# Performance work log

Measured on AMD Instinct MI355X. Metric: run time of the kernel, lower is better.

Reference implementation:

```python
import jax, jax.numpy as jnp
import numpy as np

N = 50000      # num nodes
E = 400000     # num edges (before self loops)
IN = 128       # in_channels
H = 4          # num_heads
C = 64         # hidden_channels (per head)
NEG_SLOPE = 0.2
BN_EPS = 1e-5


def gatv2_layer(x, Wl, Wr, att, bias, src, dst, n, concat):
    # GATv2Conv (PyG, share_weights=False): xl for source/messages, xr for dest
    h, c = att.shape
    xl = (x @ Wl).reshape(n, h, c)
    xr = (x @ Wr).reshape(n, h, c)
    # per-edge attention logits: [E, H]
    e = jnp.sum(jax.nn.leaky_relu(xl[src] + xr[dst], NEG_SLOPE) * att[None], axis=-1)
    # edge softmax grouped by destination node
    m = jax.ops.segment_max(e, dst, num_segments=n)          # [N, H]
    ex = jnp.exp(e - m[dst])
    den = jax.ops.segment_sum(ex, dst, num_segments=n)       # [N, H]
    alpha = ex / (den[dst] + 1e-16)                          # [E, H]
    # weighted scatter-sum aggregation: [N, H, C]
    out = jax.ops.segment_sum(alpha[..., None] * xl[src], dst, num_segments=n)
    out = out.reshape(n, h * c) if concat else out.mean(axis=1)
    return out + bias


def bn_eval(x, gamma, beta):
    # eval-mode BatchNorm1d with init running stats (mean=0, var=1)
    return x / jnp.sqrt(jnp.asarray(1.0 + BN_EPS, x.dtype)) * gamma + beta


def setup_inputs() -> dict:
    key = jax.random.key(0)
    ks = jax.random.split(key, 20)
    s = 0.05
    return {
        "x": jax.random.normal(ks[0], (N, IN), jnp.float32),
        "edge_index": jax.random.randint(ks[1], (2, E), 0, N, jnp.int32),
        # layer 1: in=128 -> heads=4, out=64, concat -> 256
        "W1l": jax.random.normal(ks[2], (IN, H * C), jnp.float32) * s,
        "W1r": jax.random.normal(ks[3], (IN, H * C), jnp.float32) * s,
        "att1": jax.random.normal(ks[4], (H, C), jnp.float32) * s,
        "b1": jnp.zeros((H * C,), jnp.float32),
        "g1": jnp.ones((H * C,), jnp.float32),
        "be1": jnp.zeros((H * C,), jnp.float32),
        # layer 2: in=256 -> heads=4, out=64, mean -> 64
        "W2l": jax.random.normal(ks[5], (H * C, H * C), jnp.float32) * s,
        "W2r": jax.random.normal(ks[6], (H * C, H * C), jnp.float32) * s,
        "att2": jax.random.normal(ks[7], (H, C), jnp.float32) * s,
        "b2": jnp.zeros((C,), jnp.float32),
        "g2": jnp.ones((C,), jnp.float32),
        "be2": jnp.zeros((C,), jnp.float32),
        # final linear 64 -> 1
        "fcW": jax.random.normal(ks[8], (C, 1), jnp.float32) * s,
        "fcb": jnp.zeros((1,), jnp.float32),
    }


def reference(x, edge_index, W1l, W1r, att1, b1, g1, be1,
              W2l, W2r, att2, b2, g2, be2, fcW, fcb):
    # PyG GATv2Conv adds self loops by default
    loops = jnp.arange(N, dtype=edge_index.dtype)
    src = jnp.concatenate([edge_index[0], loops])
    dst = jnp.concatenate([edge_index[1], loops])

    h = gatv2_layer(x, W1l, W1r, att1, b1, src, dst, N, concat=True)   # [N, 256]
    h = jax.nn.elu(bn_eval(h, g1, be1))                                 # dropout = id (eval)
    h = gatv2_layer(h, W2l, W2r, att2, b2, src, dst, N, concat=False)  # [N, 64]
    h = jax.nn.elu(bn_eval(h, g2, be2))
    out = jax.nn.sigmoid(h @ fcW + fcb)                                 # [N, 1]
    return out
```

## Files before the change

### kernel.cpp

```cpp
#include <hip/hip_runtime.h>
#include <math.h>

#define NNODES 50000
#define NEDGES 400000
#define E2 (NEDGES + NNODES)
#define HC 256
#define NOUT 512
#define NF (NOUT / 16)
#define BN_SCALE 0.9999950000374997f
#define SCAN_B ((NNODES + 255) / 256)

typedef unsigned short ushortx8 __attribute__((ext_vector_type(8)));
typedef __bf16 bf16x8 __attribute__((ext_vector_type(8)));
typedef float f32x4 __attribute__((ext_vector_type(4)));
typedef float f32x2 __attribute__((ext_vector_type(2)));

__device__ inline unsigned short f2bf(float f) {
    unsigned u = __float_as_uint(f);
    u += 0x7fff + ((u >> 16) & 1);
    return (unsigned short)(u >> 16);
}
__device__ inline float bf2f(unsigned short u) {
    return __uint_as_float(((unsigned)u) << 16);
}

__global__ void hist_dst(const int* __restrict__ ei, int* __restrict__ deg) {
    int i = blockIdx.x * blockDim.x + threadIdx.x;
    if (i >= E2) return;
    int d = (i < NEDGES) ? ei[NEDGES + i] : i - NEDGES;
    atomicAdd(&deg[d], 1);
}

__global__ __launch_bounds__(256) void scan1(const int* __restrict__ deg,
                                             int* __restrict__ rowptr,
                                             int* __restrict__ bsum) {
    int t = threadIdx.x;
    int i = blockIdx.x * 256 + t;
    int v = (i < NNODES) ? deg[i] : 0;
    __shared__ int buf[256];
    buf[t] = v;
    __syncthreads();
    for (int off = 1; off < 256; off <<= 1) {
        int u = (t >= off) ? buf[t - off] : 0;
        __syncthreads();
        buf[t] += u;
        __syncthreads();
    }
    if (i < NNODES) rowptr[i] = buf[t] - v;
    if (t == 255) bsum[blockIdx.x] = buf[255];
}

__global__ __launch_bounds__(256) void scan2(int* __restrict__ bsum,
                                             int* __restrict__ rowptr) {
    int t = threadIdx.x;
    int v = (t < SCAN_B) ? bsum[t] : 0;
    __shared__ int buf[256];
    buf[t] = v;
    __syncthreads();
    for (int off = 1; off < 256; off <<= 1) {
        int u = (t >= off) ? buf[t - off] : 0;
        __syncthreads();
        buf[t] += u;
        __syncthreads();
    }
    if (t < SCAN_B) bsum[t] = buf[t] - v;
    if (t == 0) rowptr[NNODES] = E2;
}

__global__ void scan3(int* __restrict__ rowptr, const int* __restrict__ bsum,
                      int* __restrict__ cursor) {
    int i = blockIdx.x * 256 + threadIdx.x;
    if (i >= NNODES) return;
    int r = rowptr[i] + bsum[blockIdx.x];
    rowptr[i] = r;
    cursor[i] = r;
}

__global__ void scatter_csr(const int* __restrict__ ei, int* __restrict__ cursor,
                            int* __restrict__ csr_src) {
    int i = blockIdx.x * blockDim.x + threadIdx.x;
    if (i >= E2) return;
    int s, d;
    if (i < NEDGES) { s = ei[i]; d = ei[NEDGES + i]; }
    else            { s = i - NEDGES; d = s; }
    int slot = atomicAdd(&cursor[d], 1);
    csr_src[slot] = s;
}

__device__ inline void prep_one(const float* __restrict__ Wl, const float* __restrict__ Wr,
                                unsigned short* __restrict__ Bf, int id) {
    int j    = id & 7;
    int lane = (id >> 3) & 63;
    int nf   = (id >> 9) & (NF - 1);
    int kb   = id >> 14;
    int k = kb * 32 + (lane >> 4) * 8 + j;
    int c = nf * 16 + (lane & 15);
    float v = (c < 256) ? Wl[k * 256 + c] : Wr[k * 256 + (c - 256)];
    Bf[id] = f2bf(v);
}

#define XCVT_N (NNODES * 128 / 4)
#define B1_N (128 * NOUT)
#define B2_N (256 * NOUT)

__global__ void pack_all(const float* __restrict__ x,
                         const float* __restrict__ W1l, const float* __restrict__ W1r,
                         const float* __restrict__ W2l, const float* __restrict__ W2r,
                         unsigned short* __restrict__ x_bf,
                         unsigned short* __restrict__ Bf1,
                         unsigned short* __restrict__ Bf2) {
    int id = blockIdx.x * blockDim.x + threadIdx.x;
    if (id < XCVT_N) {
        float4 v = reinterpret_cast<const float4*>(x)[id];
        ushort4 o = { f2bf(v.x), f2bf(v.y), f2bf(v.z), f2bf(v.w) };
        reinterpret_cast<ushort4*>(x_bf)[id] = o;
    } else if (id < XCVT_N + B1_N) {
        prep_one(W1l, W1r, Bf1, id - XCVT_N);
    } else if (id < XCVT_N + B1_N + B2_N) {
        prep_one(W2l, W2r, Bf2, id - XCVT_N - B1_N);
    }
}

__global__ __launch_bounds__(256) void gemm_mfma(
        const unsigned short* __restrict__ A,
        const unsigned short* __restrict__ Bf,
        unsigned short* __restrict__ C,
        int M, int K) {
    const int tid  = threadIdx.x;
    const int lane = tid & 63;
    const int w    = tid >> 6;
    const int row0 = blockIdx.x * 64;
    const int col0 = w * 128;
    const int lr = lane & 15, lg = lane >> 4;

    f32x4 acc[4][8] = {};
    const int nkb = K >> 5;
    for (int kb = 0; kb < nkb; ++kb) {
        bf16x8 af[4], bfr[8];
        const int kcol = kb * 32 + lg * 8;
#pragma unroll
        for (int i = 0; i < 4; ++i) {
            int r = row0 + i * 16 + lr;
            ushortx8 av = {};
            if (r < M)
                av = *reinterpret_cast<const ushortx8*>(A + (size_t)r * K + kcol);
            af[i] = __builtin_bit_cast(bf16x8, av);
        }
#pragma unroll
        for (int j = 0; j < 8; ++j) {
            int nf = (col0 >> 4) + j;
            ushortx8 bv = *reinterpret_cast<const ushortx8*>(
                Bf + (((size_t)(kb * NF + nf) * 64 + lane) << 3));
            bfr[j] = __builtin_bit_cast(bf16x8, bv);
        }
#pragma unroll
        for (int i = 0; i < 4; ++i)
#pragma unroll
            for (int j = 0; j < 8; ++j)
                acc[i][j] = __builtin_amdgcn_mfma_f32_16x16x32_bf16(
                    af[i], bfr[j], acc[i][j], 0, 0, 0);
    }
#pragma unroll
    for (int i = 0; i < 4; ++i) {
#pragma unroll
        for (int r = 0; r < 4; ++r) {
            int row = row0 + i * 16 + lg * 4 + r;
            if (row < M) {
#pragma unroll
                for (int j = 0; j < 8; ++j)
                    C[(size_t)row * NOUT + col0 + j * 16 + lr] = f2bf(acc[i][j][r]);
            }
        }
    }
}

template <int LAYER>
__global__ __launch_bounds__(256) void gat_node(
        const unsigned short* __restrict__ xlr,
        const float* __restrict__ att, const int* __restrict__ rowptr,
        const int* __restrict__ csr_src,
        const float* __restrict__ bias, const float* __restrict__ g,
        const float* __restrict__ be,
        const float* __restrict__ fcW, const float* __restrict__ fcb,
        void* __restrict__ outv) {
    int wid  = (blockIdx.x * blockDim.x + threadIdx.x) >> 6;
    int lane = threadIdx.x & 63;
    if (wid >= NNODES) return;

    f32x2 xb01, xb23, at01, at23;
    {
        uint2 wv = *reinterpret_cast<const uint2*>(xlr + (size_t)wid * NOUT + 256 + lane * 4);
        xb01.x = __uint_as_float(wv.x << 16);
        xb01.y = __uint_as_float(wv.x & 0xffff0000u);
        xb23.x = __uint_as_float(wv.y << 16);
        xb23.y = __uint_as_float(wv.y & 0xffff0000u);
        float4 a = *reinterpret_cast<const float4*>(att + lane * 4);
        at01.x = a.x; at01.y = a.y;
        at23.x = a.z; at23.y = a.w;
    }
    const int beg = rowptr[wid];
    const int end = rowptr[wid + 1];
    const unsigned short* __restrict__ xbase = xlr + lane * 4;

    float den = 0.f;
    f32x2 ac01 = {0.f, 0.f}, ac23 = {0.f, 0.f};

    auto edge = [&](uint2 wv) {
        f32x2 xv01, xv23;
        xv01.x = __uint_as_float(wv.x << 16);
        xv01.y = __uint_as_float(wv.x & 0xffff0000u);
        xv23.x = __uint_as_float(wv.y << 16);
        xv23.y = __uint_as_float(wv.y & 0xffff0000u);
        f32x2 v01 = xv01 + xb01;
        f32x2 v23 = xv23 + xb23;
        v01 = __builtin_elementwise_max(v01, v01 * 0.2f);
        v23 = __builtin_elementwise_max(v23, v23 * 0.2f);
        f32x2 d2 = v01 * at01 + v23 * at23;
        float part = d2.x + d2.y;
        part += __shfl_xor(part, 1);
        part += __shfl_xor(part, 2);
        part += __shfl_xor(part, 4);
        part += __shfl_xor(part, 8);
        float p = __expf(part);
        den += p;
        ac01 += p * xv01;
        ac23 += p * xv23;
    };

    int j = beg;
    for (; j + 2 <= end; j += 2) {
        int s0 = csr_src[j];
        int s1 = csr_src[j + 1];
        uint2 w0 = *reinterpret_cast<const uint2*>(xbase + (size_t)s0 * NOUT);
        uint2 w1 = *reinterpret_cast<const uint2*>(xbase + (size_t)s1 * NOUT);
        edge(w0);
        edge(w1);
    }
    if (j < end) {
        int s0 = csr_src[j];
        uint2 w0 = *reinterpret_cast<const uint2*>(xbase + (size_t)s0 * NOUT);
        edge(w0);
    }

    float inv = 1.f / (den + 1e-16f);
    float ax = ac01.x * inv, ay = ac01.y * inv, az = ac23.x * inv, aw = ac23.y * inv;

    if (LAYER == 1) {
        int c0 = lane * 4;
        float o0 = (ax + bias[c0 + 0]) * BN_SCALE * g[c0 + 0] + be[c0 + 0];
        float o1 = (ay + bias[c0 + 1]) * BN_SCALE * g[c0 + 1] + be[c0 + 1];
        float o2 = (az + bias[c0 + 2]) * BN_SCALE * g[c0 + 2] + be[c0 + 2];
        float o3 = (aw + bias[c0 + 3]) * BN_SCALE * g[c0 + 3] + be[c0 + 3];
        o0 = o0 > 0.f ? o0 : expm1f(o0);
        o1 = o1 > 0.f ? o1 : expm1f(o1);
        o2 = o2 > 0.f ? o2 : expm1f(o2);
        o3 = o3 > 0.f ? o3 : expm1f(o3);
        ushort4 o = { f2bf(o0), f2bf(o1), f2bf(o2), f2bf(o3) };
        *reinterpret_cast<ushort4*>((unsigned short*)outv + (size_t)wid * HC + lane * 4) = o;
    } else {
#pragma unroll
        for (int off = 16; off < 64; off <<= 1) {
            ax += __shfl_xor(ax, off);
            ay += __shfl_xor(ay, off);
            az += __shfl_xor(az, off);
            aw += __shfl_xor(aw, off);
        }
        int c0 = (lane & 15) * 4;
        float v0 = (ax * 0.25f + bias[c0 + 0]) * BN_SCALE * g[c0 + 0] + be[c0 + 0];
        float v1 = (ay * 0.25f + bias[c0 + 1]) * BN_SCALE * g[c0 + 1] + be[c0 + 1];
        float v2 = (az * 0.25f + bias[c0 + 2]) * BN_SCALE * g[c0 + 2] + be[c0 + 2];
        float v3 = (aw * 0.25f + bias[c0 + 3]) * BN_SCALE * g[c0 + 3] + be[c0 + 3];
        v0 = v0 > 0.f ? v0 : expm1f(v0);
        v1 = v1 > 0.f ? v1 : expm1f(v1);
        v2 = v2 > 0.f ? v2 : expm1f(v2);
        v3 = v3 > 0.f ? v3 : expm1f(v3);
        float dot = v0 * fcW[c0] + v1 * fcW[c0 + 1] + v2 * fcW[c0 + 2] + v3 * fcW[c0 + 3];
#pragma unroll
        for (int off = 8; off; off >>= 1) dot += __shfl_xor(dot, off);
        if (lane == 0) ((float*)outv)[wid] = 1.f / (1.f + __expf(-(dot + fcb[0])));
    }
}

extern "C" void kernel_launch(void* const* d_in, const int* in_sizes, int n_in,
                              void* d_out, int out_size, void* d_ws, size_t ws_size,
                              hipStream_t stream) {
    const float* x    = (const float*)d_in[0];
    const int*   ei   = (const int*)d_in[1];
    const float* W1l  = (const float*)d_in[2];
    const float* W1r  = (const float*)d_in[3];
    const float* att1 = (const float*)d_in[4];
    const float* b1   = (const float*)d_in[5];
    const float* g1   = (const float*)d_in[6];
    const float* be1  = (const float*)d_in[7];
    const float* W2l  = (const float*)d_in[8];
    const float* W2r  = (const float*)d_in[9];
    const float* att2 = (const float*)d_in[10];
    const float* b2   = (const float*)d_in[11];
    const float* g2   = (const float*)d_in[12];
    const float* be2  = (const float*)d_in[13];
    const float* fcW  = (const float*)d_in[14];
    const float* fcb  = (const float*)d_in[15];
    float* out = (float*)d_out;

    unsigned short* xlr   = (unsigned short*)d_ws;
    unsigned short* x_bf  = xlr + (size_t)NNODES * NOUT;
    unsigned short* h1_bf = x_bf + (size_t)NNODES * 128;
    unsigned short* Bf1   = h1_bf + (size_t)NNODES * 256;
    unsigned short* Bf2   = Bf1 + 128 * NOUT;
    int* csr_src = (int*)(Bf2 + 256 * NOUT);
    int* deg     = csr_src + E2;
    int* rowptr  = deg + NNODES;
    int* cursor  = rowptr + NNODES + 1;
    int* bsum    = cursor + NNODES;

    const int edgeBlocks = (E2 + 255) / 256;
    const int nodeBlocks = (NNODES * 64 + 255) / 256;
    const int gemmGrid   = (NNODES + 63) / 64;
    const int packBlocks = (XCVT_N + B1_N + B2_N + 255) / 256;

    hipMemsetAsync(deg, 0, NNODES * sizeof(int), stream);
    hist_dst<<<edgeBlocks, 256, 0, stream>>>(ei, deg);
    scan1<<<SCAN_B, 256, 0, stream>>>(deg, rowptr, bsum);
    scan2<<<1, 256, 0, stream>>>(bsum, rowptr);
    scan3<<<SCAN_B, 256, 0, stream>>>(rowptr, bsum, cursor);
    scatter_csr<<<edgeBlocks, 256, 0, stream>>>(ei, cursor, csr_src);

    pack_all<<<packBlocks, 256, 0, stream>>>(x, W1l, W1r, W2l, W2r, x_bf, Bf1, Bf2);

    gemm_mfma<<<gemmGrid, 256, 0, stream>>>(x_bf, Bf1, xlr, NNODES, 128);
    gat_node<1><<<nodeBlocks, 256, 0, stream>>>(xlr, att1, rowptr, csr_src,
                                                b1, g1, be1, nullptr, nullptr, h1_bf);

    gemm_mfma<<<gemmGrid, 256, 0, stream>>>(h1_bf, Bf2, xlr, NNODES, 256);
    gat_node<2><<<nodeBlocks, 256, 0, stream>>>(xlr, att2, rowptr, csr_src,
                                                b2, g2, be2, fcW, fcb, out);
}
```

Measured before the change: 232.9 us.

## Fuse CSR build into pack/GEMM launches, use DPP reductions, unroll edge loop by 4

Merges the histogram into the pack kernel and the first scan pass into the first GEMM launch using block-index dispatch. It also replaces the separate scan2/scan3 kernels with a single kernel in which each block reduces its preceding block sums. This cuts the number of launches and serial gaps in the setup phase. Separately, it replaces the shuffle-based 16-lane reductions in the GAT node kernels with DPP row operations and unrolls the edge gather loop to four edges for more memory-level parallelism. The costs are higher register pressure and some redundant per-block summation in the scan.

Measured after the change: 208.9 us. 1.11x faster.

```diff
diff --git a/kernel.cpp b/kernel.cpp
--- a/kernel.cpp
+++ b/kernel.cpp
@@ -9,6 +9,8 @@
 #define NF (NOUT / 16)
 #define BN_SCALE 0.9999950000374997f
 #define SCAN_B ((NNODES + 255) / 256)
+#define GEMM_B ((NNODES + 63) / 64)
+#define HIST_B ((E2 + 255) / 256)
 
 typedef unsigned short ushortx8 __attribute__((ext_vector_type(8)));
 typedef __bf16 bf16x8 __attribute__((ext_vector_type(8)));
@@ -20,75 +22,28 @@
     u += 0x7fff + ((u >> 16) & 1);
     return (unsigned short)(u >> 16);
 }
-__device__ inline float bf2f(unsigned short u) {
-    return __uint_as_float(((unsigned)u) << 16);
-}
-
-__global__ void hist_dst(const int* __restrict__ ei, int* __restrict__ deg) {
-    int i = blockIdx.x * blockDim.x + threadIdx.x;
-    if (i >= E2) return;
-    int d = (i < NEDGES) ? ei[NEDGES + i] : i - NEDGES;
-    atomicAdd(&deg[d], 1);
-}
-
-__global__ __launch_bounds__(256) void scan1(const int* __restrict__ deg,
-                                             int* __restrict__ rowptr,
-                                             int* __restrict__ bsum) {
-    int t = threadIdx.x;
-    int i = blockIdx.x * 256 + t;
-    int v = (i < NNODES) ? deg[i] : 0;
-    __shared__ int buf[256];
-    buf[t] = v;
-    __syncthreads();
-    for (int off = 1; off < 256; off <<= 1) {
-        int u = (t >= off) ? buf[t - off] : 0;
-        __syncthreads();
-        buf[t] += u;
-        __syncthreads();
-    }
-    if (i < NNODES) rowptr[i] = buf[t] - v;
-    if (t == 255) bsum[blockIdx.x] = buf[255];
-}
-
-__global__ __launch_bounds__(256) void scan2(int* __restrict__ bsum,
-                                             int* __restrict__ rowptr) {
-    int t = threadIdx.x;
-    int v = (t < SCAN_B) ? bsum[t] : 0;
-    __shared__ int buf[256];
-    buf[t] = v;
-    __syncthreads();
-    for (int off = 1; off < 256; off <<= 1) {
-        int u = (t >= off) ? buf[t - off] : 0;
-        __syncthreads();
-        buf[t] += u;
-        __syncthreads();
-    }
-    if (t < SCAN_B) bsum[t] = buf[t] - v;
-    if (t == 0) rowptr[NNODES] = E2;
-}
-
-__global__ void scan3(int* __restrict__ rowptr, const int* __restrict__ bsum,
-                      int* __restrict__ cursor) {
-    int i = blockIdx.x * 256 + threadIdx.x;
-    if (i >= NNODES) return;
-    int r = rowptr[i] + bsum[blockIdx.x];
-    rowptr[i] = r;
-    cursor[i] = r;
-}
-
-__global__ void scatter_csr(const int* __restrict__ ei, int* __restrict__ cursor,
-                            int* __restrict__ csr_src) {
-    int i = blockIdx.x * blockDim.x + threadIdx.x;
-    if (i >= E2) return;
-    int s, d;
-    if (i < NEDGES) { s = ei[i]; d = ei[NEDGES + i]; }
-    else            { s = i - NEDGES; d = s; }
-    int slot = atomicAdd(&cursor[d], 1);
-    csr_src[slot] = s;
-}
-
-__device__ inline void prep_one(const float* __restrict__ Wl, const float* __restrict__ Wr,
-                                unsigned short* __restrict__ Bf, int id) {
+
+template <int CTRL>
+__device__ __forceinline__ float dpp_add(float x) {
+    int y = __builtin_amdgcn_update_dpp(0, __float_as_int(x), CTRL, 0xF, 0xF, true);
+    return x + __int_as_float(y);
+}
+__device__ __forceinline__ float row16_sum(float x) {
+    x = dpp_add<0xB1>(x);
+    x = dpp_add<0x4E>(x);
+    x = dpp_add<0x141>(x);
+    x = dpp_add<0x140>(x);
+    return x;
+}
+
+#define XCVT_N (NNODES * 128 / 4)
+#define B1_N (128 * NOUT)
+#define B2_N (256 * NOUT)
+#define PACK_B ((XCVT_N + B1_N + B2_N + 255) / 256)
+
+__device__ __forceinline__ void prep_one(const float* __restrict__ Wl,
+                                         const float* __restrict__ Wr,
+                                         unsigned short* __restrict__ Bf, int id) {
     int j    = id & 7;
     int lane = (id >> 3) & 63;
     int nf   = (id >> 9) & (NF - 1);
@@ -99,37 +54,40 @@
     Bf[id] = f2bf(v);
 }
 
-#define XCVT_N (NNODES * 128 / 4)
-#define B1_N (128 * NOUT)
-#define B2_N (256 * NOUT)
-
-__global__ void pack_all(const float* __restrict__ x,
-                         const float* __restrict__ W1l, const float* __restrict__ W1r,
-                         const float* __restrict__ W2l, const float* __restrict__ W2r,
-                         unsigned short* __restrict__ x_bf,
-                         unsigned short* __restrict__ Bf1,
-                         unsigned short* __restrict__ Bf2) {
-    int id = blockIdx.x * blockDim.x + threadIdx.x;
-    if (id < XCVT_N) {
-        float4 v = reinterpret_cast<const float4*>(x)[id];
-        ushort4 o = { f2bf(v.x), f2bf(v.y), f2bf(v.z), f2bf(v.w) };
-        reinterpret_cast<ushort4*>(x_bf)[id] = o;
-    } else if (id < XCVT_N + B1_N) {
-        prep_one(W1l, W1r, Bf1, id - XCVT_N);
-    } else if (id < XCVT_N + B1_N + B2_N) {
-        prep_one(W2l, W2r, Bf2, id - XCVT_N - B1_N);
-    }
-}
-
-__global__ __launch_bounds__(256) void gemm_mfma(
-        const unsigned short* __restrict__ A,
-        const unsigned short* __restrict__ Bf,
-        unsigned short* __restrict__ C,
-        int M, int K) {
-    const int tid  = threadIdx.x;
+__global__ __launch_bounds__(256) void k1_pack_hist(
+        const float* __restrict__ x,
+        const float* __restrict__ W1l, const float* __restrict__ W1r,
+        const float* __restrict__ W2l, const float* __restrict__ W2r,
+        unsigned short* __restrict__ x_bf,
+        unsigned short* __restrict__ Bf1, unsigned short* __restrict__ Bf2,
+        const int* __restrict__ ei, int* __restrict__ deg) {
+    int bid = blockIdx.x;
+    if (bid < PACK_B) {
+        int id = bid * 256 + threadIdx.x;
+        if (id < XCVT_N) {
+            float4 v = reinterpret_cast<const float4*>(x)[id];
+            ushort4 o = { f2bf(v.x), f2bf(v.y), f2bf(v.z), f2bf(v.w) };
+            reinterpret_cast<ushort4*>(x_bf)[id] = o;
+        } else if (id < XCVT_N + B1_N) {
+            prep_one(W1l, W1r, Bf1, id - XCVT_N);
+        } else if (id < XCVT_N + B1_N + B2_N) {
+            prep_one(W2l, W2r, Bf2, id - XCVT_N - B1_N);
+        }
+    } else {
+        int i = (bid - PACK_B) * 256 + threadIdx.x;
+        if (i < E2) {
+            int d = (i < NEDGES) ? ei[NEDGES + i] : i - NEDGES;
+            atomicAdd(&deg[d], 1);
+        }
+    }
+}
+
+__device__ __forceinline__ void gemm_body(int bx, int tid,
+        const unsigned short* __restrict__ A, const unsigned short* __restrict__ Bf,
+        unsigned short* __restrict__ C, int M, int K) {
     const int lane = tid & 63;
     const int w    = tid >> 6;
-    const int row0 = blockIdx.x * 64;
+    const int row0 = bx * 64;
     const int col0 = w * 128;
     const int lr = lane & 15, lg = lane >> 4;
 
@@ -172,6 +130,69 @@
             }
         }
     }
+}
+
+__global__ __launch_bounds__(256) void k2_gemm1_scan1(
+        const unsigned short* __restrict__ A, const unsigned short* __restrict__ Bf,
+        unsigned short* __restrict__ C, int M, int K,
+        const int* __restrict__ deg, int* __restrict__ rowptr, int* __restrict__ bsum) {
+    __shared__ int buf[256];
+    if (blockIdx.x < GEMM_B) {
+        gemm_body(blockIdx.x, threadIdx.x, A, Bf, C, M, K);
+    } else {
+        int bx = blockIdx.x - GEMM_B;
+        int t = threadIdx.x;
+        int i = bx * 256 + t;
+        int v = (i < NNODES) ? deg[i] : 0;
+        buf[t] = v;
+        __syncthreads();
+        for (int off = 1; off < 256; off <<= 1) {
+            int u = (t >= off) ? buf[t - off] : 0;
+            __syncthreads();
+            buf[t] += u;
+            __syncthreads();
+        }
+        if (i < NNODES) rowptr[i] = buf[t] - v;
+        if (t == 255) bsum[bx] = buf[255];
+    }
+}
+
+__global__ __launch_bounds__(256) void k3_scan23(
+        const int* __restrict__ bsum, int* __restrict__ rowptr, int* __restrict__ cursor) {
+    __shared__ int sbuf[256];
+    int t = threadIdx.x;
+    int v = (t < (int)blockIdx.x && t < SCAN_B) ? bsum[t] : 0;
+    sbuf[t] = v;
+    __syncthreads();
+    for (int off = 128; off; off >>= 1) {
+        if (t < off) sbuf[t] += sbuf[t + off];
+        __syncthreads();
+    }
+    int base = sbuf[0];
+    int i = blockIdx.x * 256 + t;
+    if (i < NNODES) {
+        int r = rowptr[i] + base;
+        rowptr[i] = r;
+        cursor[i] = r;
+    }
+    if (blockIdx.x == 0 && t == 0) rowptr[NNODES] = E2;
+}
+
+__global__ __launch_bounds__(256) void k4_scatter(
+        const int* __restrict__ ei, int* __restrict__ cursor, int* __restrict__ csr_src) {
+    int i = blockIdx.x * blockDim.x + threadIdx.x;
+    if (i >= E2) return;
+    int s, d;
+    if (i < NEDGES) { s = ei[i]; d = ei[NEDGES + i]; }
+    else            { s = i - NEDGES; d = s; }
+    int slot = atomicAdd(&cursor[d], 1);
+    csr_src[slot] = s;
+}
+
+__global__ __launch_bounds__(256) void gemm_mfma(
+        const unsigned short* __restrict__ A, const unsigned short* __restrict__ Bf,
+        unsigned short* __restrict__ C, int M, int K) {
+    gemm_body(blockIdx.x, threadIdx.x, A, Bf, C, M, K);
 }
 
 template <int LAYER>
@@ -216,11 +237,7 @@
         v01 = __builtin_elementwise_max(v01, v01 * 0.2f);
         v23 = __builtin_elementwise_max(v23, v23 * 0.2f);
         f32x2 d2 = v01 * at01 + v23 * at23;
-        float part = d2.x + d2.y;
-        part += __shfl_xor(part, 1);
-        part += __shfl_xor(part, 2);
-        part += __shfl_xor(part, 4);
-        part += __shfl_xor(part, 8);
+        float part = row16_sum(d2.x + d2.y);
         float p = __expf(part);
         den += p;
         ac01 += p * xv01;
@@ -228,15 +245,15 @@
     };
 
     int j = beg;
-    for (; j + 2 <= end; j += 2) {
-        int s0 = csr_src[j];
-        int s1 = csr_src[j + 1];
+    for (; j + 4 <= end; j += 4) {
+        int s0 = csr_src[j], s1 = csr_src[j + 1], s2 = csr_src[j + 2], s3 = csr_src[j + 3];
         uint2 w0 = *reinterpret_cast<const uint2*>(xbase + (size_t)s0 * NOUT);
         uint2 w1 = *reinterpret_cast<const uint2*>(xbase + (size_t)s1 * NOUT);
-        edge(w0);
-        edge(w1);
-    }
-    if (j < end) {
+        uint2 w2 = *reinterpret_cast<const uint2*>(xbase + (size_t)s2 * NOUT);
+        uint2 w3 = *reinterpret_cast<const uint2*>(xbase + (size_t)s3 * NOUT);
+        edge(w0); edge(w1); edge(w2); edge(w3);
+    }
+    for (; j < end; ++j) {
         int s0 = csr_src[j];
         uint2 w0 = *reinterpret_cast<const uint2*>(xbase + (size_t)s0 * NOUT);
         edge(w0);
@@ -275,8 +292,7 @@
         v2 = v2 > 0.f ? v2 : expm1f(v2);
         v3 = v3 > 0.f ? v3 : expm1f(v3);
         float dot = v0 * fcW[c0] + v1 * fcW[c0 + 1] + v2 * fcW[c0 + 2] + v3 * fcW[c0 + 3];
-#pragma unroll
-        for (int off = 8; off; off >>= 1) dot += __shfl_xor(dot, off);
+        dot = row16_sum(dot);
         if (lane == 0) ((float*)outv)[wid] = 1.f / (1.f + __expf(-(dot + fcb[0])));
     }
 }
@@ -313,25 +329,24 @@
     int* cursor  = rowptr + NNODES + 1;
     int* bsum    = cursor + NNODES;
 
-    const int edgeBlocks = (E2 + 255) / 256;
     const int nodeBlocks = (NNODES * 64 + 255) / 256;
-    const int gemmGrid   = (NNODES + 63) / 64;
-    const int packBlocks = (XCVT_N + B1_N + B2_N + 255) / 256;
 
     hipMemsetAsync(deg, 0, NNODES * sizeof(int), stream);
-    hist_dst<<<edgeBlocks, 256, 0, stream>>>(ei, deg);
-    scan1<<<SCAN_B, 256, 0, stream>>>(deg, rowptr, bsum);
-    scan2<<<1, 256, 0, stream>>>(bsum, rowptr);
-    scan3<<<SCAN_B, 256, 0, stream>>>(rowptr, bsum, cursor);
-    scatter_csr<<<edgeBlocks, 256, 0, stream>>>(ei, cursor, csr_src);
-
-    pack_all<<<packBlocks, 256, 0, stream>>>(x, W1l, W1r, W2l, W2r, x_bf, Bf1, Bf2);
-
-    gemm_mfma<<<gemmGrid, 256, 0, stream>>>(x_bf, Bf1, xlr, NNODES, 128);
+
+    k1_pack_hist<<<PACK_B + HIST_B, 256, 0, stream>>>(
+        x, W1l, W1r, W2l, W2r, x_bf, Bf1, Bf2, ei, deg);
+
+    k2_gemm1_scan1<<<GEMM_B + SCAN_B, 256, 0, stream>>>(
+        x_bf, Bf1, xlr, NNODES, 128, deg, rowptr, bsum);
+
+    k3_scan23<<<SCAN_B, 256, 0, stream>>>(bsum, rowptr, cursor);
+
+    k4_scatter<<<HIST_B, 256, 0, stream>>>(ei, cursor, csr_src);
+
     gat_node<1><<<nodeBlocks, 256, 0, stream>>>(xlr, att1, rowptr, csr_src,
                                                 b1, g1, be1, nullptr, nullptr, h1_bf);
 
-    gemm_mfma<<<gemmGrid, 256, 0, stream>>>(h1_bf, Bf2, xlr, NNODES, 256);
+    gemm_mfma<<<GEMM_B, 256, 0, stream>>>(h1_bf, Bf2, xlr, NNODES, 256);
     gat_node<2><<<nodeBlocks, 256, 0, stream>>>(xlr, att2, rowptr, csr_src,
                                                 b2, g2, be2, fcW, fcb, out);
 }
```
